# Performance work log

Hardware: AMD Instinct MI355X
Metric: run time of the kernel (lower is better)

Reference implementation:

```python
import jax, jax.numpy as jnp
import numpy as np
from math import sqrt

B, L, S, H, E = 4, 2048, 2048, 8, 64
T = 1.0  # softmax temperature


def setup_inputs() -> dict:
    key = jax.random.key(0)
    kq, kk, kv = jax.random.split(key, 3)
    q = jax.random.normal(kq, (B, L, H, E), dtype=jnp.float32)
    k = jax.random.normal(kk, (B, S, H, E), dtype=jnp.float32)
    v = jax.random.normal(kv, (B, S, H, E), dtype=jnp.float32)
    mask = jnp.zeros((B, L), dtype=jnp.bool_)  # unused by the module, kept for signature fidelity
    return {"q": q, "k": k, "v": v, "mask": mask}


def reference(q, k, v, mask):
    Bq, Lq, Hq, Eq = q.shape
    # [B,L,H,E] -> [B,H,E,L]; FFT over time axis
    xq = jnp.transpose(q, (0, 2, 3, 1))
    xk = jnp.transpose(k, (0, 2, 3, 1))
    xv = jnpp_t = jnp.transpose(v, (0, 2, 3, 1))
    xq_ft = jnp.fft.rfft(xq, axis=-1, norm='ortho')   # [B,H,E,Lf]
    xk_ft = jnp.fft.rfft(xk, axis=-1, norm='ortho')   # [B,H,E,Sf]
    xv_ft = jnp.fft.rfft(xv, axis=-1, norm='ortho')   # [B,H,E,Sf]
    # complex frequency-domain scores [B,H,Lf,Sf]
    scores = jnp.einsum('bhex,bhey->bhxy', xq_ft, jnp.conj(xk_ft)) / sqrt(Eq)
    # activation == 'softmax': softmax over |scores|/T, then real-weighted complex mix
    attn = jax.nn.softmax(jnp.abs(scores) / T, axis=-1)
    xqkv_ft = jnp.einsum('bhxy,bhey->bhex', attn.astype(xv_ft.dtype), xv_ft)  # [B,H,E,Lf]
    out = jnp.fft.irfft(xqkv_ft, n=Lq, axis=-1, norm='ortho')  # [B,H,E,L]
    return jnp.transpose(out, (0, 3, 1, 2))  # [B,L,H,E]
```

## Files before the change

kernel.cpp:

```cpp
#include <hip/hip_runtime.h>
#include <hip/hip_bf16.h>
#include <math.h>

#define LOGN  11
#define NN    2048
#define LOGM  10
#define MM    1024
#define NF    1025
#define NYP   1056
#define TWO_PI 6.283185307179586f
#define INV_SQRT_N 0.022097086912079608f
#define INV_SCALE  0.044194173824159216f

typedef __attribute__((ext_vector_type(8))) short bhalf8;
typedef __attribute__((ext_vector_type(4))) float f32x4;

#define MFMA16(a, b, c) __builtin_amdgcn_mfma_f32_16x16x32_bf16(a, b, c, 0, 0, 0)

#define GLD16(gp, lp)                                                              \
    __builtin_amdgcn_global_load_lds(                                              \
        (const __attribute__((address_space(1))) void*)(gp),                       \
        (__attribute__((address_space(3))) void*)(lp), 16, 0, 0)

#define CVTPK(dst, lo, hi) \
    asm("v_cvt_pk_bf16_f32 %0, %1, %2" : "=v"(dst) : "v"(lo), "v"(hi))

__device__ __forceinline__ unsigned short f2bf(float f) {
    union { float f; unsigned u; } v; v.f = f;
    unsigned r = v.u + 0x7FFFu + ((v.u >> 16) & 1u);
    return (unsigned short)(r >> 16);
}
__device__ __forceinline__ float bf2f(unsigned short h) {
    union { unsigned u; float f; } v; v.u = ((unsigned)h) << 16;
    return v.f;
}

__device__ __forceinline__ void fft_stages_m(float2* buf, const float2* tw, int tid)
{
    for (int st = 1; st <= LOGM; st++) {
        int half = 1 << (st - 1);
        #pragma unroll
        for (int it = 0; it < 2; it++) {
            int j   = tid + 256 * it;
            int pos = j & (half - 1);
            int grp = j >> (st - 1);
            int i0  = (grp << st) + pos;
            int i1  = i0 + half;
            float2 w = tw[pos << (LOGM - st)];
            float2 a = buf[i0];
            float2 b = buf[i1];
            float2 bw = make_float2(b.x * w.x - b.y * w.y,
                                    b.x * w.y + b.y * w.x);
            buf[i0] = make_float2(a.x + bw.x, a.y + bw.y);
            buf[i1] = make_float2(a.x - bw.x, a.y - bw.y);
        }
        __syncthreads();
    }
}

__global__ __launch_bounds__(256) void tr_fwd(const float* __restrict__ q,
                                              const float* __restrict__ k,
                                              const float* __restrict__ v,
                                              unsigned short* __restrict__ ttr)
{
    __shared__ float Ts[64][65];
    int tt     = blockIdx.x;
    int h      = blockIdx.y;
    int z      = blockIdx.z;
    int tensor = z >> 2;
    int b      = z & 3;
    int tid    = threadIdx.x;
    int t0     = tt * 64;

    const float* in = (tensor == 0) ? q : (tensor == 1) ? k : v;

    {
        int tl = tid >> 2, ec = (tid & 3) * 16;
        const float* src = in + ((size_t)b * 2048 + t0 + tl) * 512 + h * 64 + ec;
        #pragma unroll
        for (int m = 0; m < 4; m++) {
            float4 v4 = *(const float4*)(src + m * 4);
            Ts[tl][ec + m * 4 + 0] = v4.x;
            Ts[tl][ec + m * 4 + 1] = v4.y;
            Ts[tl][ec + m * 4 + 2] = v4.z;
            Ts[tl][ec + m * 4 + 3] = v4.w;
        }
    }
    __syncthreads();
    {
        int el = tid >> 2, tc = (tid & 3) * 16;
        size_t row = ((size_t)(tensor * 32 + b * 8 + h)) * 64 + el;
        unsigned short* dst = ttr + row * 2048 + t0 + tc;
        #pragma unroll
        for (int m = 0; m < 4; m++) {
            float a0 = Ts[tc + m * 4 + 0][el], a1 = Ts[tc + m * 4 + 1][el];
            float a2 = Ts[tc + m * 4 + 2][el], a3 = Ts[tc + m * 4 + 3][el];
            unsigned u0, u1;
            CVTPK(u0, a0, a1);
            CVTPK(u1, a2, a3);
            uint2 o; o.x = u0; o.y = u1;
            *(uint2*)(dst + m * 4) = o;
        }
    }
}

__global__ __launch_bounds__(256) void fft_fwd(const unsigned short* __restrict__ ttr,
                                               unsigned short* __restrict__ Pq,
                                               unsigned short* __restrict__ Pk,
                                               unsigned short* __restrict__ Pv)
{
    __shared__ float2 buf[MM];
    __shared__ float2 tw[MM / 2];

    int g      = blockIdx.x;
    int p      = g % 96;
    int e      = g / 96;
    int tensor = p / 32;
    int bh     = p % 32;
    int tid    = threadIdx.x;

    unsigned short* plane = (tensor == 0) ? Pq : (tensor == 1) ? Pk : Pv;
    float scl = (tensor == 0) ? (INV_SQRT_N * 0.125f) : INV_SQRT_N;
    int vk3 = (tensor == 2) ? (((e >> 2) & 3) << 3) : 0;

    for (int i = tid; i < MM / 2; i += 256) {
        float ang = -TWO_PI * (float)i / (float)MM;
        float sv, cv;
        __sincosf(ang, &sv, &cv);
        tw[i] = make_float2(cv, sv);
    }

    const unsigned short* src = ttr + ((size_t)p * 64 + e) * 2048;
    #pragma unroll
    for (int i = 0; i < 4; i++) {
        int j = tid + 256 * i;
        unsigned pr = *(const unsigned*)(src + 2 * j);
        float x0 = bf2f((unsigned short)(pr & 0xFFFFu));
        float x1 = bf2f((unsigned short)(pr >> 16));
        buf[__brev((unsigned)j) >> (32 - LOGM)] = make_float2(x0, x1);
    }
    __syncthreads();

    fft_stages_m(buf, tw, tid);

    unsigned short* dre = plane + ((size_t)bh * 128 + e) * NYP;
    unsigned short* dim_ = dre + (size_t)64 * NYP;

#define RPOINT(Ai, Bi, KKi, XR, XI) do {                                   \
        float Ex = 0.5f * (Ai.x + Bi.x), Ey = 0.5f * (Ai.y - Bi.y);        \
        float Dx = 0.5f * (Ai.x - Bi.x), Dy = 0.5f * (Ai.y + Bi.y);        \
        float Ox = Dy, Oy = -Dx;                                           \
        float th = -(TWO_PI / (float)NN) * (float)(KKi);                   \
        float sn, cs; __sincosf(th, &sn, &cs);                             \
        XR = (Ex + cs * Ox - sn * Oy) * scl;                               \
        XI = (Ey + cs * Oy + sn * Ox) * scl;                               \
    } while (0)

    #pragma unroll
    for (int i = 0; i < 2; i++) {
        int kk = 2 * tid + 512 * i;
        float2 A0 = buf[kk];
        float2 B0 = buf[(MM - kk) & (MM - 1)];
        float2 A1 = buf[kk + 1];
        float2 B1 = buf[MM - kk - 1];
        float Xr0, Xi0, Xr1, Xi1;
        RPOINT(A0, B0, kk, Xr0, Xi0);
        RPOINT(A1, B1, kk + 1, Xr1, Xi1);
        unsigned ur, ui;
        CVTPK(ur, Xr0, Xr1);
        CVTPK(ui, Xi0, Xi1);
        int ks = kk ^ vk3;
        *(unsigned*)(dre + ks)  = ur;
        *(unsigned*)(dim_ + ks) = ui;
    }
    if (tid < 16) {
        unsigned ur = 0, ui = 0;
        if (tid == 0) {
            float2 A = buf[0];
            float sn, cs;
            __sincosf(-(TWO_PI / (float)NN) * 1024.0f, &sn, &cs);
            float Xr = (A.x + cs * A.y) * scl;
            float Xi = (sn * A.y) * scl;
            float zz = 0.f;
            CVTPK(ur, Xr, zz);
            CVTPK(ui, Xi, zz);
        }
        int ks = (1024 + 2 * tid) ^ vk3;
        *(unsigned*)(dre + ks)  = ur;
        *(unsigned*)(dim_ + ks) = ui;
    }
#undef RPOINT
}

__global__ __launch_bounds__(256) void qkpack(const unsigned short* __restrict__ Pq,
                                              const unsigned short* __restrict__ Pk,
                                              unsigned short* __restrict__ Qp,
                                              unsigned short* __restrict__ Kp)
{
    __shared__ unsigned short Ts[32][136];
    int y0  = blockIdx.x * 32;
    int bh  = blockIdx.y;
    int tsr = blockIdx.z;
    int tid = threadIdx.x;

    const unsigned short* srcp = (tsr == 0) ? Pq : Pk;
    unsigned short* dstp       = (tsr == 0) ? Qp : Kp;

    {
        int kk = tid >> 1, seg = tid & 1;
        const unsigned short* sp = srcp + ((size_t)bh * 128 + kk) * NYP + y0 + seg * 16;
        uint4 va = *(const uint4*)sp;
        uint4 vb = *(const uint4*)(sp + 8);
        const unsigned short* pa = (const unsigned short*)&va;
        const unsigned short* pb = (const unsigned short*)&vb;
        #pragma unroll
        for (int j = 0; j < 8; j++) Ts[seg * 16 + j][kk] = pa[j];
        #pragma unroll
        for (int j = 0; j < 8; j++) Ts[seg * 16 + 8 + j][kk] = pb[j];
    }
    __syncthreads();
    {
        int y = tid >> 3, c = tid & 7;
        uint4 lo = *(const uint4*)&Ts[y][c * 16];
        uint4 hi = *(const uint4*)&Ts[y][c * 16 + 8];
        char* rowb = (char*)(dstp + ((size_t)bh * NYP + y0 + y) * 128);
        if (tsr == 0) {
            *(uint4*)(rowb + c * 32)      = lo;
            *(uint4*)(rowb + c * 32 + 16) = hi;
        } else {
            int s = y & 7;
            *(uint4*)(rowb + (((2 * c)     ^ s) << 4)) = lo;
            *(uint4*)(rowb + (((2 * c + 1) ^ s) << 4)) = hi;
        }
    }
}

struct FlashShared {
    union {
        struct {
            unsigned short Ks[2][32][128];
            unsigned short Vs[2][128][32];
        } kv;
        unsigned short OutT[128][72];
    } u;
    unsigned short Ps[4][16][40];
};

__global__ __launch_bounds__(256) void flash_mfma(
    const unsigned short* __restrict__ Qp,
    const unsigned short* __restrict__ Kp,
    const unsigned short* __restrict__ Vt,
    unsigned short* __restrict__ numb,
    float* __restrict__ lbuf)
{
    __shared__ FlashShared S;

    int g    = blockIdx.x;
    int bh   = g & 31;
    int idx  = g >> 5;
    int half = idx / 17;
    int x0   = (idx % 17) * 64;
    int tid  = threadIdx.x;
    int w    = tid >> 6;
    int lane = tid & 63;
    int qd   = lane >> 4;
    int col  = lane & 15;

    int xrow = x0 + w * 16 + col;
    int xq   = min(xrow, 1024);
    const unsigned short* qb = Qp + ((size_t)bh * NYP + xq) * 128 + qd * 8;
    bhalf8 Are[4], Aim[4];
    #pragma unroll
    for (int ks = 0; ks < 4; ks++) Are[ks] = *(const bhalf8*)(qb + ks * 32);
    Aim[0] = Are[2];
    Aim[1] = Are[3];
    #pragma unroll
    for (int ks = 0; ks < 2; ks++) {
        bhalf8 t = Are[ks];
        unsigned* u = (unsigned*)&t;
        #pragma unroll
        for (int j = 0; j < 4; j++) u[j] ^= 0x80008000u;
        Aim[ks + 2] = t;
    }

    f32x4 O[8];
    #pragma unroll
    for (int n = 0; n < 8; n++) O[n] = (f32x4){0.f, 0.f, 0.f, 0.f};
    float Lacc[4] = {0.f, 0.f, 0.f, 0.f};

    int yt0 = half * 17, yt1 = min(33, yt0 + 17);

    const char* ksrc = (const char*)Kp
        + ((size_t)bh * NYP + (size_t)yt0 * 32 + w * 8) * 256 + lane * 16;
    const char* vbase = (const char*)Vt + (size_t)bh * 128 * (NYP * 2);
    const char* vsrc0 = vbase + ((size_t)(w * 32) + (lane >> 2)) * (NYP * 2)
                        + (size_t)yt0 * 64 + (lane & 3) * 16;
    const char* vsrc1 = vsrc0 + (size_t)16 * (NYP * 2);

    int sw = col & 7;
    int kco[4];
    #pragma unroll
    for (int ks = 0; ks < 4; ks++) kco[ks] = ((ks * 4 + qd) ^ sw) * 8;
    int vq = (qd ^ ((col >> 2) & 3)) * 8;

    {
        int pb = yt0 & 1;
        GLD16(ksrc,         &S.u.kv.Ks[pb][w * 8][0]);
        GLD16(ksrc + 1024,  &S.u.kv.Ks[pb][w * 8 + 4][0]);
        GLD16(vsrc0,        &S.u.kv.Vs[pb][w * 32][0]);
        GLD16(vsrc1,        &S.u.kv.Vs[pb][w * 32 + 16][0]);
        ksrc += 8192; vsrc0 += 64; vsrc1 += 64;
    }

    for (int yt = yt0; yt < yt1; yt++) {
        int cb = yt & 1, nb = cb ^ 1;
        if (yt + 1 < yt1) {
            GLD16(ksrc,         &S.u.kv.Ks[nb][w * 8][0]);
            GLD16(ksrc + 1024,  &S.u.kv.Ks[nb][w * 8 + 4][0]);
            GLD16(vsrc0,        &S.u.kv.Vs[nb][w * 32][0]);
            GLD16(vsrc1,        &S.u.kv.Vs[nb][w * 32 + 16][0]);
            ksrc += 8192; vsrc0 += 64; vsrc1 += 64;
            __builtin_amdgcn_sched_barrier(0);
            asm volatile("s_waitcnt vmcnt(4)" ::: "memory");
        } else {
            __builtin_amdgcn_sched_barrier(0);
            asm volatile("s_waitcnt vmcnt(0)" ::: "memory");
        }
        __builtin_amdgcn_sched_barrier(0);
        __builtin_amdgcn_s_barrier();
        __builtin_amdgcn_sched_barrier(0);

        const unsigned short* k0 = &S.u.kv.Ks[cb][col][0];
        const unsigned short* k1 = &S.u.kv.Ks[cb][col + 16][0];

        f32x4 sre[2], sim[2];
        #pragma unroll
        for (int sc = 0; sc < 2; sc++) {
            sre[sc] = (f32x4){0.f, 0.f, 0.f, 0.f};
            sim[sc] = (f32x4){0.f, 0.f, 0.f, 0.f};
        }
        __builtin_amdgcn_s_setprio(1);
        #pragma unroll
        for (int ks = 0; ks < 4; ks++) {
            bhalf8 b0 = *(const bhalf8*)(k0 + kco[ks]);
            bhalf8 b1 = *(const bhalf8*)(k1 + kco[ks]);
            sre[0] = MFMA16(Are[ks], b0, sre[0]);
            sim[0] = MFMA16(Aim[ks], b0, sim[0]);
            sre[1] = MFMA16(Are[ks], b1, sre[1]);
            sim[1] = MFMA16(Aim[ks], b1, sim[1]);
        }
        __builtin_amdgcn_s_setprio(0);

        #pragma unroll
        for (int r = 0; r < 4; r++) {
            float re0 = sre[0][r], im0 = sim[0][r];
            float re1 = sre[1][r], im1 = sim[1][r];
            float p0 = __expf(__builtin_amdgcn_sqrtf(fmaf(re0, re0, im0 * im0)));
            float p1 = __expf(__builtin_amdgcn_sqrtf(fmaf(re1, re1, im1 * im1)));
            Lacc[r] += p0 + p1;
            unsigned up;
            CVTPK(up, p0, p1);
            S.Ps[w][qd * 4 + r][col]      = (unsigned short)up;
            S.Ps[w][qd * 4 + r][col + 16] = (unsigned short)(up >> 16);
        }

        bhalf8 pa = *(const bhalf8*)&S.Ps[w][col][qd * 8];
        __builtin_amdgcn_s_setprio(1);
        #pragma unroll
        for (int n = 0; n < 8; n++) {
            bhalf8 bv = *(const bhalf8*)&S.u.kv.Vs[cb][n * 16 + col][vq];
            O[n] = MFMA16(pa, bv, O[n]);
        }
        __builtin_amdgcn_s_setprio(0);

        asm volatile("s_waitcnt lgkmcnt(0)" ::: "memory");
        __builtin_amdgcn_sched_barrier(0);
        __builtin_amdgcn_s_barrier();
        __builtin_amdgcn_sched_barrier(0);
    }

    size_t hofs = (size_t)half * 32 * NYP;
    #pragma unroll
    for (int r = 0; r < 4; r++) {
        float ls = Lacc[r];
        ls += __shfl_xor(ls, 1);
        ls += __shfl_xor(ls, 2);
        ls += __shfl_xor(ls, 4);
        ls += __shfl_xor(ls, 8);
        if (half == 1) ls -= 31.0f;
        int x = x0 + w * 16 + qd * 4 + r;
        if (x <= 1024 && col == 0) lbuf[hofs + (size_t)bh * NYP + x] = ls;
    }

    __syncthreads();
    #pragma unroll
    for (int n = 0; n < 8; n++) {
        unsigned u0, u1;
        CVTPK(u0, O[n][0], O[n][1]);
        CVTPK(u1, O[n][2], O[n][3]);
        *(unsigned*)&S.u.OutT[n * 16 + col][w * 16 + qd * 4]     = u0;
        *(unsigned*)&S.u.OutT[n * 16 + col][w * 16 + qd * 4 + 2] = u1;
    }
    __syncthreads();
    {
        int kk2 = tid >> 1, seg = tid & 1;
        int xg  = x0 + seg * 32;
        if (xg < NYP) {
            unsigned short* dst =
                numb + (((size_t)half * 32 + bh) * 128 + kk2) * NYP + xg;
            const unsigned short* srcl = &S.u.OutT[kk2][seg * 32];
            #pragma unroll
            for (int m = 0; m < 4; m++)
                *(uint4*)(dst + m * 8) = *(const uint4*)(srcl + m * 8);
        }
    }
}

__global__ __launch_bounds__(256) void fft_inv(const unsigned short* __restrict__ numb,
                                               const float* __restrict__ lbuf,
                                               float* __restrict__ st)
{
    __shared__ float2 buf[MM];
    __shared__ float2 tw[MM / 2];

    int s   = blockIdx.x;
    int e   = s & 63;
    int bh  = s >> 6;
    int tid = threadIdx.x;

    for (int i = tid; i < MM / 2; i += 256) {
        float ang = TWO_PI * (float)i / (float)MM;
        float sv, cv;
        __sincosf(ang, &sv, &cv);
        tw[i] = make_float2(cv, sv);
    }

    const size_t HS = (size_t)32 * 128 * NYP;
    const unsigned short* nbr = numb + ((size_t)bh * 128 + e) * NYP;
    const unsigned short* nbi = numb + ((size_t)bh * 128 + 64 + e) * NYP;
    const float* l0 = lbuf + (size_t)bh * NYP;
    const float* l1 = l0 + (size_t)32 * NYP;

    #pragma unroll
    for (int i = 0; i < 4; i++) {
        int kk = tid + 256 * i;
        int x1 = kk, x2 = 1024 - kk;
        float iv1 = 1.f / (l0[x1] + l1[x1]);
        float iv2 = 1.f / (l0[x2] + l1[x2]);
        float Ax = (bf2f(nbr[x1]) + bf2f(nbr[HS + x1])) * iv1;
        float Ay = (bf2f(nbi[x1]) + bf2f(nbi[HS + x1])) * iv1;
        float Bx = (bf2f(nbr[x2]) + bf2f(nbr[HS + x2])) * iv2;
        float By = -((bf2f(nbi[x2]) + bf2f(nbi[HS + x2])) * iv2);
        float Ex = 0.5f * (Ax + Bx), Ey = 0.5f * (Ay + By);
        float Dx = 0.5f * (Ax - Bx), Dy = 0.5f * (Ay - By);
        float th = (TWO_PI / (float)NN) * (float)kk;
        float sn, cs;
        __sincosf(th, &sn, &cs);
        float Ox = Dx * cs - Dy * sn;
        float Oy = Dx * sn + Dy * cs;
        buf[__brev((unsigned)kk) >> (32 - LOGM)] = make_float2(Ex - Oy, Ey + Ox);
    }
    __syncthreads();

    fft_stages_m(buf, tw, tid);

    float* dst = st + ((size_t)bh * 64 + e) * 2048;
    #pragma unroll
    for (int i = 0; i < 4; i++) {
        int j = tid + 256 * i;
        float2 z = buf[j];
        *(float2*)&dst[2 * j] = make_float2(z.x * INV_SCALE, z.y * INV_SCALE);
    }
}

__global__ __launch_bounds__(256) void out_tr(const float* __restrict__ st,
                                              float* __restrict__ out)
{
    __shared__ float Ts[64][65];
    int tt  = blockIdx.x;
    int h   = blockIdx.y;
    int b   = blockIdx.z;
    int tid = threadIdx.x;
    int bh  = b * 8 + h;

    {
        int e = tid >> 2, tc = (tid & 3) * 16;
        const float* src = st + ((size_t)bh * 64 + e) * 2048 + tt * 64 + tc;
        #pragma unroll
        for (int m = 0; m < 4; m++) {
            float4 v4 = *(const float4*)(src + m * 4);
            Ts[e][tc + m * 4 + 0] = v4.x;
            Ts[e][tc + m * 4 + 1] = v4.y;
            Ts[e][tc + m * 4 + 2] = v4.z;
            Ts[e][tc + m * 4 + 3] = v4.w;
        }
    }
    __syncthreads();
    {
        int t = tid >> 2, ec = (tid & 3) * 16;
        float* dst = out + (size_t)b * 2048 * 512 + (size_t)(tt * 64 + t) * 512
                     + h * 64 + ec;
        #pragma unroll
        for (int m = 0; m < 4; m++) {
            float4 v4;
            v4.x = Ts[ec + m * 4 + 0][t];
            v4.y = Ts[ec + m * 4 + 1][t];
            v4.z = Ts[ec + m * 4 + 2][t];
            v4.w = Ts[ec + m * 4 + 3][t];
            *(float4*)(dst + m * 4) = v4;
        }
    }
}

extern "C" void kernel_launch(void* const* d_in, const int* in_sizes, int n_in,
                              void* d_out, int out_size, void* d_ws, size_t ws_size,
                              hipStream_t stream)
{
    const float* q = (const float*)d_in[0];
    const float* k = (const float*)d_in[1];
    const float* v = (const float*)d_in[2];
    float* out = (float*)d_out;

    char* ws = (char*)d_ws;
    const size_t PL = (size_t)32 * 128 * NYP * sizeof(unsigned short);
    unsigned short* Pq = (unsigned short*)(ws);
    unsigned short* Pk = (unsigned short*)(ws + PL);
    unsigned short* Pv = (unsigned short*)(ws + 2 * PL);
    unsigned short* ttr = (unsigned short*)(ws + 3 * PL);
    unsigned short* Qp = (unsigned short*)(ws + 3 * PL);
    unsigned short* Kp = (unsigned short*)(ws + 4 * PL);
    unsigned short* numb = (unsigned short*)(ws);
    float* st   = (float*)(ws + 3 * PL);
    float* lbuf = (float*)(ws + 5 * PL);

    hipLaunchKernelGGL(tr_fwd, dim3(32, 8, 12), dim3(256), 0, stream,
                       q, k, v, ttr);
    hipLaunchKernelGGL(fft_fwd, dim3(3 * 2048), dim3(256), 0, stream,
                       ttr, Pq, Pk, Pv);
    hipLaunchKernelGGL(qkpack, dim3(33, 32, 2), dim3(256), 0, stream,
                       Pq, Pk, Qp, Kp);
    hipLaunchKernelGGL(flash_mfma, dim3(1088), dim3(256), 0, stream,
                       Qp, Kp, Pv, numb, lbuf);
    hipLaunchKernelGGL(fft_inv, dim3(2048), dim3(256), 0, stream,
                       numb, lbuf, st);
    hipLaunchKernelGGL(out_tr, dim3(32, 8, 4), dim3(256), 0, stream,
                       st, out);
}
```

Measured before the change: 216.5 us.

## Split flash key range into four chunks and use native exp2 with prescaled Q

When the workspace is large enough, the flash attention kernel splits the key axis into four chunks instead of two. This doubles the block count to 2176 for better CU occupancy. The fft_inv kernel then sums four partial numerators and denominators. Separately, Q is prescaled by log2(e) so the softmax exponent can use a raw v_exp_f32 instead of __expf. The trade-off is more partial-result memory traffic and extra reduction work in fft_inv.

```diff
diff --git a/kernel.cpp b/kernel.cpp
--- a/kernel.cpp
+++ b/kernel.cpp
@@ -11,6 +11,7 @@
 #define TWO_PI 6.283185307179586f
 #define INV_SQRT_N 0.022097086912079608f
 #define INV_SCALE  0.044194173824159216f
+#define LOG2E      1.4426950408889634f
 
 typedef __attribute__((ext_vector_type(8))) short bhalf8;
 typedef __attribute__((ext_vector_type(4))) float f32x4;
@@ -24,6 +25,9 @@
 
 #define CVTPK(dst, lo, hi) \
     asm("v_cvt_pk_bf16_f32 %0, %1, %2" : "=v"(dst) : "v"(lo), "v"(hi))
+
+#define EXP2F(dst, src) \
+    asm("v_exp_f32 %0, %1" : "=v"(dst) : "v"(src))
 
 __device__ __forceinline__ unsigned short f2bf(float f) {
     union { float f; unsigned u; } v; v.f = f;
@@ -120,7 +124,7 @@
     int tid    = threadIdx.x;
 
     unsigned short* plane = (tensor == 0) ? Pq : (tensor == 1) ? Pk : Pv;
-    float scl = (tensor == 0) ? (INV_SQRT_N * 0.125f) : INV_SQRT_N;
+    float scl = (tensor == 0) ? (INV_SQRT_N * 0.125f * LOG2E) : INV_SQRT_N;
     int vk3 = (tensor == 2) ? (((e >> 2) & 3) << 3) : 0;
 
     for (int i = tid; i < MM / 2; i += 256) {
@@ -246,11 +250,13 @@
     unsigned short Ps[4][16][40];
 };
 
+template<int NH>
 __global__ __launch_bounds__(256) void flash_mfma(
     const unsigned short* __restrict__ Qp,
     const unsigned short* __restrict__ Kp,
     const unsigned short* __restrict__ Vt,
-    unsigned short* __restrict__ numb,
+    unsigned short* __restrict__ nb0,
+    unsigned short* __restrict__ nb1,
     float* __restrict__ lbuf)
 {
     __shared__ FlashShared S;
@@ -288,7 +294,7 @@
     for (int n = 0; n < 8; n++) O[n] = (f32x4){0.f, 0.f, 0.f, 0.f};
     float Lacc[4] = {0.f, 0.f, 0.f, 0.f};
 
-    int yt0 = half * 17, yt1 = min(33, yt0 + 17);
+    int yt0 = (half * 33) / NH, yt1 = ((half + 1) * 33) / NH;
 
     const char* ksrc = (const char*)Kp
         + ((size_t)bh * NYP + (size_t)yt0 * 32 + w * 8) * 256 + lane * 16;
@@ -355,8 +361,11 @@
         for (int r = 0; r < 4; r++) {
             float re0 = sre[0][r], im0 = sim[0][r];
             float re1 = sre[1][r], im1 = sim[1][r];
-            float p0 = __expf(__builtin_amdgcn_sqrtf(fmaf(re0, re0, im0 * im0)));
-            float p1 = __expf(__builtin_amdgcn_sqrtf(fmaf(re1, re1, im1 * im1)));
+            float s0 = __builtin_amdgcn_sqrtf(fmaf(re0, re0, im0 * im0));
+            float s1 = __builtin_amdgcn_sqrtf(fmaf(re1, re1, im1 * im1));
+            float p0, p1;
+            EXP2F(p0, s0);
+            EXP2F(p1, s1);
             Lacc[r] += p0 + p1;
             unsigned up;
             CVTPK(up, p0, p1);
@@ -379,7 +388,6 @@
         __builtin_amdgcn_sched_barrier(0);
     }
 
-    size_t hofs = (size_t)half * 32 * NYP;
     #pragma unroll
     for (int r = 0; r < 4; r++) {
         float ls = Lacc[r];
@@ -387,10 +395,14 @@
         ls += __shfl_xor(ls, 2);
         ls += __shfl_xor(ls, 4);
         ls += __shfl_xor(ls, 8);
-        if (half == 1) ls -= 31.0f;
+        if (yt1 == 33) ls -= 31.0f;
         int x = x0 + w * 16 + qd * 4 + r;
-        if (x <= 1024 && col == 0) lbuf[hofs + (size_t)bh * NYP + x] = ls;
-    }
+        if (x <= 1024 && col == 0)
+            lbuf[((size_t)half * 32 + bh) * NYP + x] = ls;
+    }
+
+    const size_t HSZ = (size_t)32 * 128 * NYP;
+    unsigned short* nplane = (half < 2 ? nb0 : nb1) + (size_t)(half & 1) * HSZ;
 
     __syncthreads();
     #pragma unroll
@@ -406,8 +418,7 @@
         int kk2 = tid >> 1, seg = tid & 1;
         int xg  = x0 + seg * 32;
         if (xg < NYP) {
-            unsigned short* dst =
-                numb + (((size_t)half * 32 + bh) * 128 + kk2) * NYP + xg;
+            unsigned short* dst = nplane + ((size_t)bh * 128 + kk2) * NYP + xg;
             const unsigned short* srcl = &S.u.OutT[kk2][seg * 32];
             #pragma unroll
             for (int m = 0; m < 4; m++)
@@ -416,7 +427,9 @@
     }
 }
 
-__global__ __launch_bounds__(256) void fft_inv(const unsigned short* __restrict__ numb,
+template<int NH>
+__global__ __launch_bounds__(256) void fft_inv(const unsigned short* __restrict__ nb0,
+                                               const unsigned short* __restrict__ nb1,
                                                const float* __restrict__ lbuf,
                                                float* __restrict__ st)
 {
@@ -435,22 +448,36 @@
         tw[i] = make_float2(cv, sv);
     }
 
-    const size_t HS = (size_t)32 * 128 * NYP;
-    const unsigned short* nbr = numb + ((size_t)bh * 128 + e) * NYP;
-    const unsigned short* nbi = numb + ((size_t)bh * 128 + 64 + e) * NYP;
-    const float* l0 = lbuf + (size_t)bh * NYP;
-    const float* l1 = l0 + (size_t)32 * NYP;
+    const size_t HSZ = (size_t)32 * 128 * NYP;
+    const unsigned short* pre[NH];
+    const unsigned short* pim[NH];
+    const float* lb[NH];
+    #pragma unroll
+    for (int h = 0; h < NH; h++) {
+        const unsigned short* base = (h < 2 ? nb0 : nb1) + (size_t)(h & 1) * HSZ;
+        pre[h] = base + ((size_t)bh * 128 + e) * NYP;
+        pim[h] = base + ((size_t)bh * 128 + 64 + e) * NYP;
+        lb[h]  = lbuf + ((size_t)h * 32 + bh) * NYP;
+    }
 
     #pragma unroll
     for (int i = 0; i < 4; i++) {
         int kk = tid + 256 * i;
         int x1 = kk, x2 = 1024 - kk;
-        float iv1 = 1.f / (l0[x1] + l1[x1]);
-        float iv2 = 1.f / (l0[x2] + l1[x2]);
-        float Ax = (bf2f(nbr[x1]) + bf2f(nbr[HS + x1])) * iv1;
-        float Ay = (bf2f(nbi[x1]) + bf2f(nbi[HS + x1])) * iv1;
-        float Bx = (bf2f(nbr[x2]) + bf2f(nbr[HS + x2])) * iv2;
-        float By = -((bf2f(nbi[x2]) + bf2f(nbi[HS + x2])) * iv2);
+        float d1 = 0.f, d2 = 0.f;
+        float Axs = 0.f, Ays = 0.f, Bxs = 0.f, Bys = 0.f;
+        #pragma unroll
+        for (int h = 0; h < NH; h++) {
+            d1 += lb[h][x1];
+            d2 += lb[h][x2];
+            Axs += bf2f(pre[h][x1]);
+            Ays += bf2f(pim[h][x1]);
+            Bxs += bf2f(pre[h][x2]);
+            Bys += bf2f(pim[h][x2]);
+        }
+        float iv1 = 1.f / d1, iv2 = 1.f / d2;
+        float Ax = Axs * iv1, Ay = Ays * iv1;
+        float Bx = Bxs * iv2, By = -(Bys * iv2);
         float Ex = 0.5f * (Ax + Bx), Ey = 0.5f * (Ay + By);
         float Dx = 0.5f * (Ax - Bx), Dy = 0.5f * (Ay - By);
         float th = (TWO_PI / (float)NN) * (float)kk;
@@ -529,9 +556,10 @@
     unsigned short* ttr = (unsigned short*)(ws + 3 * PL);
     unsigned short* Qp = (unsigned short*)(ws + 3 * PL);
     unsigned short* Kp = (unsigned short*)(ws + 4 * PL);
-    unsigned short* numb = (unsigned short*)(ws);
-    float* st   = (float*)(ws + 3 * PL);
-    float* lbuf = (float*)(ws + 5 * PL);
+    float* st = (float*)(ws + 3 * PL);
+
+    const size_t lbuf4 = (size_t)4 * 32 * NYP * sizeof(float);
+    bool big = ws_size >= 7 * PL + lbuf4;
 
     hipLaunchKernelGGL(tr_fwd, dim3(32, 8, 12), dim3(256), 0, stream,
                        q, k, v, ttr);
@@ -539,10 +567,24 @@
                        ttr, Pq, Pk, Pv);
     hipLaunchKernelGGL(qkpack, dim3(33, 32, 2), dim3(256), 0, stream,
                        Pq, Pk, Qp, Kp);
-    hipLaunchKernelGGL(flash_mfma, dim3(1088), dim3(256), 0, stream,
-                       Qp, Kp, Pv, numb, lbuf);
-    hipLaunchKernelGGL(fft_inv, dim3(2048), dim3(256), 0, stream,
-                       numb, lbuf, st);
+
+    if (big) {
+        unsigned short* nb0 = (unsigned short*)(ws);
+        unsigned short* nb1 = (unsigned short*)(ws + 5 * PL);
+        float* lbuf = (float*)(ws + 7 * PL);
+        hipLaunchKernelGGL((flash_mfma<4>), dim3(17 * 4 * 32), dim3(256), 0, stream,
+                           Qp, Kp, Pv, nb0, nb1, lbuf);
+        hipLaunchKernelGGL((fft_inv<4>), dim3(2048), dim3(256), 0, stream,
+                           nb0, nb1, lbuf, st);
+    } else {
+        unsigned short* nb0 = (unsigned short*)(ws);
+        float* lbuf = (float*)(ws + 5 * PL);
+        hipLaunchKernelGGL((flash_mfma<2>), dim3(17 * 2 * 32), dim3(256), 0, stream,
+                           Qp, Kp, Pv, nb0, nb0, lbuf);
+        hipLaunchKernelGGL((fft_inv<2>), dim3(2048), dim3(256), 0, stream,
+                           nb0, nb0, lbuf, st);
+    }
+
     hipLaunchKernelGGL(out_tr, dim3(32, 8, 4), dim3(256), 0, stream,
                        st, out);
 }
```

After: 215.8 us. No clear change (-0.3%).
